# Performance work log

Hardware: AMD Instinct MI355X
Metric: run time of the kernel (lower is better)

The kernel has to match this reference:

```python
import jax, jax.numpy as jnp
import numpy as np

# PercentClosenessBoosting (not in provided source): standard form is
#   new_boost = boost_tensor + (1 - tensor / tensor.max()) * boost_percent
# i.e. units far from the max get boosted more.

def _fwd_math(x, boost_tensor, sparsity, boost_percent):
    B, E = x.shape
    # --- run_boosting ---
    new_boost = boost_tensor + (1.0 - x / jnp.max(x)) * boost_percent
    boosted = jnp.maximum(x, 0.0) + new_boost
    # inhibition tensor starts empty -> apply_sparse_self_affector is a no-op
    # --- run_k_winners_positive: top-k (max_active) per row of boosted, binarize ---
    order = jnp.argsort(-boosted, axis=1)          # descending sort indices
    rank = jnp.argsort(order, axis=1)              # rank of each element in its row
    max_active = jnp.ceil(sparsity[1] * E)
    saved = jnp.where((rank < max_active) & (boosted > 0), 1.0, 0.0)  # ctx.save_for_backward
    # --- choose_boosted_to_satisfy_minimum (note: GLOBAL sum vs per-row min, faithful) ---
    min_active = jnp.floor(sparsity[0] * E)
    active = jnp.sum(saved)
    to_activate = jnp.ceil(min_active - active)
    border = jnp.argsort(-new_boost, axis=1)
    brank = jnp.argsort(border, axis=1)
    need = active < min_active
    out = jnp.where(need & (brank < to_activate), 1.0, saved)
    # --- zero boost where active ---
    final_boost = jnp.where(out > 0, jnp.zeros_like(new_boost), new_boost)
    return out, final_boost, saved


def setup_inputs() -> dict:
    key = jax.random.key(0)
    k1, = jax.random.split(key, 1)
    B, E = 64, 131072
    x = jax.random.normal(k1, (B, E), dtype=jnp.float32)
    boost_tensor = jnp.zeros((B, E), dtype=jnp.float32)
    sparsity = jnp.array([0.002, 0.02], dtype=jnp.float32)
    boost_percent = jnp.float32(1e-8)
    return {"x": x, "boost_tensor": boost_tensor, "sparsity": sparsity, "boost_percent": boost_percent}


def reference(x, boost_tensor, sparsity, boost_percent):
    out, final_boost, _ = _fwd_math(x, boost_tensor, sparsity, boost_percent)
    return out, final_boost
```

## Files before the change

### kernel.cpp

```cpp
#include <hip/hip_runtime.h>

#define BR 64
#define EC 131072
#define CAP 8192
#define LCAP 1024
#define CHUNKS 16
#define CHUNK_V (EC / CHUNKS / 4)
#define NSCH 41
#define NS (NSCH * 64)
#define SSTRIDE 3197
#define BINS 4096

typedef float nf4 __attribute__((ext_vector_type(4)));

#define WS_GMAX 0
#define WS_TOACT 2
#define WS_UT 136
#define WS_CUT 200
#define WS_CCNT 264
#define WS_UT2 512
#define WS_CUT2 576
#define WS_NPOS 640
#define WS_BMAX 1024
#define CAND_U_OFF 4096
#define CAND_I_OFF (CAND_U_OFF + BR * CAP)

__device__ __forceinline__ unsigned map_f(float f) {
    unsigned b = __float_as_uint(f);
    return (b & 0x80000000u) ? ~b : (b | 0x80000000u);
}
__device__ __forceinline__ float unmap_f(unsigned u) {
    unsigned b = (u & 0x80000000u) ? (u & 0x7FFFFFFFu) : ~u;
    return __uint_as_float(b);
}

__device__ __forceinline__ void compute_vals(float x, float bt, float gmax, float bp,
                                             float* nb, float* bo) {
#pragma clang fp contract(off)
    float q = x / gmax;
    float t = 1.0f - q;
    float p = t * bp;
    float nbv = bt + p;
    *nb = nbv;
    *bo = fmaxf(x, 0.0f) + nbv;
}

__device__ __forceinline__ unsigned umax_(unsigned a, unsigned b) { return a > b ? a : b; }
__device__ __forceinline__ unsigned umin_(unsigned a, unsigned b) { return a < b ? a : b; }

__device__ __forceinline__ unsigned calc_K(const float* sp) {
    unsigned K = (unsigned)ceilf(sp[1] * (float)EC);
    if (K > EC) K = EC;
    if (K == 0) K = 1;
    return K;
}

__device__ unsigned lds_radix_select(const unsigned* su, unsigned n, unsigned K,
                                     unsigned* hist, unsigned* scan, unsigned* sb,
                                     int t, unsigned* krem) {
    unsigned pv = 0, Kp = K;
    for (int pass = 0; pass < 4; ++pass) {
        int shift = 24 - 8 * pass;
        hist[t] = 0;
        __syncthreads();
        for (unsigned i = t; i < n; i += 256) {
            unsigned u = su[i];
            bool match = (pass == 0) || ((u >> (shift + 8)) == (pv >> (shift + 8)));
            if (match) atomicAdd(&hist[(u >> shift) & 0xFFu], 1u);
        }
        __syncthreads();
        unsigned my = hist[t];
        scan[t] = my;
        __syncthreads();
        for (int off = 1; off < 256; off <<= 1) {
            unsigned v = (t + off < 256) ? scan[t + off] : 0u;
            __syncthreads();
            scan[t] += v;
            __syncthreads();
        }
        unsigned incl = scan[t], excl = incl - my;
        if (excl < Kp && incl >= Kp) {
            sb[0] = pv | ((unsigned)t << shift);
            sb[1] = Kp - excl;
        }
        __syncthreads();
        pv = sb[0];
        Kp = sb[1];
        __syncthreads();
    }
    *krem = Kp;
    return pv;
}

template<int USE_NB>
__device__ unsigned row_select_full(const float* xr, const float* br, float gmax,
                                    float bp, unsigned K, unsigned* hist,
                                    unsigned* aux, int t,
                                    unsigned* ut_out, unsigned* cut_out) {
    unsigned prefix = 0, Kp = K;
    for (int pass = 0; pass < 4; ++pass) {
        int shift = 24 - 8 * pass;
        hist[t] = 0;
        __syncthreads();
        for (int i = t; i < EC; i += 256) {
            float nb, bo;
            compute_vals(xr[i], br[i], gmax, bp, &nb, &bo);
            unsigned u = map_f(USE_NB ? nb : bo);
            bool match = (pass == 0) || ((u >> (shift + 8)) == (prefix >> (shift + 8)));
            if (match) atomicAdd(&hist[(u >> shift) & 0xFFu], 1u);
        }
        __syncthreads();
        if (t == 0) {
            unsigned cum = 0, bsel = 0, kr = Kp;
            for (int b = 255; b >= 0; --b) {
                unsigned h = hist[b];
                if (cum + h >= Kp) { bsel = (unsigned)b; kr = Kp - cum; break; }
                cum += h;
            }
            aux[0] = prefix | (bsel << shift);
            aux[1] = kr;
        }
        __syncthreads();
        prefix = aux[0];
        Kp = aux[1];
        __syncthreads();
    }
    unsigned u_t = prefix, ties = Kp;
    if (t == 0) { aux[6] = 0; aux[7] = 0xFFFFFFFFu; }
    __syncthreads();
    int wid = t >> 6, lane = t & 63;
    for (int base0 = 0; base0 < EC; base0 += 256) {
        int i = base0 + t;
        float nb, bo;
        compute_vals(xr[i], br[i], gmax, bp, &nb, &bo);
        bool eq = (map_f(USE_NB ? nb : bo) == u_t);
        unsigned long long bal = __ballot(eq);
        if (lane == 0) aux[2 + wid] = (unsigned)__popcll(bal);
        __syncthreads();
        unsigned run = aux[6];
        unsigned wpre = 0;
        for (int w = 0; w < wid; ++w) wpre += aux[2 + w];
        if (eq) {
            unsigned r = run + wpre + (unsigned)__popcll(bal & ((1ull << lane) - 1ull));
            if (r == ties - 1) aux[7] = (unsigned)i;
        }
        __syncthreads();
        if (t == 0) aux[6] = run + aux[2] + aux[3] + aux[4] + aux[5];
        __syncthreads();
        if (aux[6] >= ties) break;
    }
    if (t == 0) { *ut_out = u_t; *cut_out = aux[7]; }
    __syncthreads();
    return u_t;
}

__global__ __launch_bounds__(256) void kA(const float4* __restrict__ x4,
                                          unsigned* __restrict__ ws) {
    if (blockIdx.x == 0)
        for (int i = threadIdx.x; i < 1024; i += 256) ws[i] = 0u;
    unsigned m = 0;
    const int nvec = BR * EC / 4;
    int stride = gridDim.x * 256;
    for (int v = blockIdx.x * 256 + threadIdx.x; v < nvec; v += stride) {
        float4 xv = x4[v];
        m = umax_(m, map_f(xv.x)); m = umax_(m, map_f(xv.y));
        m = umax_(m, map_f(xv.z)); m = umax_(m, map_f(xv.w));
    }
    for (int off = 32; off; off >>= 1) m = umax_(m, __shfl_down(m, off, 64));
    __shared__ unsigned sm[4];
    if ((threadIdx.x & 63) == 0) sm[threadIdx.x >> 6] = m;
    __syncthreads();
    if (threadIdx.x == 0)
        ws[WS_BMAX + blockIdx.x] = umax_(umax_(sm[0], sm[1]), umax_(sm[2], sm[3]));
}

__global__ __launch_bounds__(256) void kB(const float* __restrict__ x,
                                          const float* __restrict__ bt,
                                          const float* __restrict__ sp,
                                          const float* __restrict__ bp_p,
                                          unsigned* __restrict__ ws) {
    __shared__ unsigned hist[BINS];
    __shared__ unsigned lu[LCAP], li[LCAP];
    __shared__ unsigned ssum[256], sabove[256];
    __shared__ unsigned sred[4];
    __shared__ unsigned stlo, slcnt, sgbase;
    int t = threadIdx.x;
    int row = blockIdx.x >> 4, chunk = blockIdx.x & (CHUNKS - 1);

    unsigned m = 0;
    for (int i = t; i < 1024; i += 256) m = umax_(m, ws[WS_BMAX + i]);
    for (int off = 32; off; off >>= 1) m = umax_(m, __shfl_down(m, off, 64));
    if ((t & 63) == 0) sred[t >> 6] = m;
    __syncthreads();
    unsigned gmu = umax_(umax_(sred[0], sred[1]), umax_(sred[2], sred[3]));
    if (blockIdx.x == 0 && t == 0) ws[WS_GMAX] = gmu;
    float gmax = unmap_f(gmu);
    float bp = *bp_p;

    for (int i = t; i < BINS; i += 256) hist[i] = 0;
    if (t == 0) slcnt = 0;
    __syncthreads();
    const float* xr = x + (size_t)row * EC;
    const float* br = bt + (size_t)row * EC;
    for (int s = t; s < NS; s += 256) {
        int idx = (s >> 6) * SSTRIDE + (s & 63);
        float nb, bo;
        compute_vals(xr[idx], br[idx], gmax, bp, &nb, &bo);
        atomicAdd(&hist[map_f(bo) >> 20], 1u);
    }
    __syncthreads();

    unsigned K = calc_K(sp);
    unsigned R = (unsigned)ceilf(1.75f * (float)NS * (float)K / (float)EC);
    if (R < 32) R = 32;
    if (R > NS) R = NS;
    unsigned hv[16];
    unsigned s = 0;
    #pragma unroll
    for (int j = 0; j < 16; ++j) { hv[j] = hist[t * 16 + j]; s += hv[j]; }
    ssum[t] = s;
    __syncthreads();
    if (t == 0) {
        unsigned acc = 0;
        for (int q = 255; q >= 0; --q) { sabove[q] = acc; acc += ssum[q]; }
    }
    __syncthreads();
    unsigned cum = sabove[t];
    for (int j = 15; j >= 0; --j) {
        unsigned h = hv[j];
        if (cum < R && cum + h >= R) stlo = ((unsigned)(t * 16 + j)) << 20;
        cum += h;
    }
    __syncthreads();
    unsigned tlo = stlo ? stlo - 1u : 0u;

    const float4* x4 = (const float4*)x;
    const float4* bt4 = (const float4*)bt;
    unsigned* cu = ws + CAND_U_OFF + (size_t)row * CAP;
    unsigned* ci = ws + CAND_I_OFF + (size_t)row * CAP;
    size_t base = (size_t)row * (EC / 4) + (size_t)chunk * CHUNK_V;
    int ebase = chunk * (EC / CHUNKS);
    unsigned posc = 0;
    for (int v = t; v < CHUNK_V; v += 256) {
        float4 xv = x4[base + v];
        float4 bv = bt4[base + v];
        float xs[4] = {xv.x, xv.y, xv.z, xv.w};
        float bs[4] = {bv.x, bv.y, bv.z, bv.w};
        #pragma unroll
        for (int j = 0; j < 4; ++j) {
            float nb, bo;
            compute_vals(xs[j], bs[j], gmax, bp, &nb, &bo);
            unsigned u = map_f(bo);
            posc += (u > 0x80000000u) ? 1u : 0u;
            if (u > tlo) {
                unsigned p = atomicAdd(&slcnt, 1u);
                if (p < LCAP) {
                    lu[p] = u; li[p] = (unsigned)(ebase + v * 4 + j);
                } else {
                    unsigned gp = atomicAdd(&ws[WS_CCNT + row], 1u);
                    if (gp < CAP) { cu[gp] = u; ci[gp] = (unsigned)(ebase + v * 4 + j); }
                }
            }
        }
    }
    for (int off = 32; off; off >>= 1) posc += __shfl_down(posc, off, 64);
    if ((t & 63) == 0) sred[t >> 6] = posc;
    __syncthreads();
    if (t == 0) atomicAdd(&ws[WS_NPOS + row], sred[0] + sred[1] + sred[2] + sred[3]);
    __syncthreads();
    unsigned n = slcnt < LCAP ? slcnt : LCAP;
    if (t == 0) sgbase = atomicAdd(&ws[WS_CCNT + row], n);
    __syncthreads();
    unsigned gb = sgbase;
    for (unsigned i = t; i < n; i += 256) {
        unsigned gp = gb + i;
        if (gp < CAP) { cu[gp] = lu[i]; ci[gp] = li[i]; }
    }
}

__global__ __launch_bounds__(256) void kC(const float* __restrict__ x,
                                          const float* __restrict__ bt,
                                          const float* __restrict__ sp,
                                          const float* __restrict__ bp_p,
                                          unsigned* __restrict__ ws) {
    int row = blockIdx.x;
    int t = threadIdx.x;
    unsigned n = ws[WS_CCNT + row];
    unsigned K = calc_K(sp);
    float gmax = unmap_f(ws[WS_GMAX]);
    float bp = *bp_p;
    __shared__ unsigned su[CAP];
    __shared__ unsigned hist[256], scan[256], sb[2];
    __shared__ unsigned marr[256];
    __shared__ unsigned mcnt;
    __shared__ unsigned aux[8];
    __shared__ unsigned sact;
    if (n >= K && n <= CAP) {
        const unsigned* cu = ws + CAND_U_OFF + (size_t)row * CAP;
        const unsigned* ci = ws + CAND_I_OFF + (size_t)row * CAP;
        for (unsigned i = t; i < n; i += 256) su[i] = cu[i];
        if (t == 0) mcnt = 0;
        __syncthreads();
        unsigned krem2;
        unsigned u_t = lds_radix_select(su, n, K, hist, scan, sb, t, &krem2);
        for (unsigned i = t; i < n; i += 256)
            if (su[i] == u_t) {
                unsigned p = atomicAdd(&mcnt, 1u);
                if (p < 256) marr[p] = ci[i];
            }
        __syncthreads();
        unsigned m = mcnt;
        if (m <= 256) {
            for (unsigned i = t; i < m; i += 256) {
                unsigned myidx = marr[i];
                unsigned r = 0;
                for (unsigned j = 0; j < m; ++j) r += (marr[j] < myidx) ? 1u : 0u;
                if (r == krem2 - 1) { ws[WS_UT + row] = u_t; ws[WS_CUT + row] = myidx; }
            }
        } else {
            for (unsigned i = t; i < n; i += 256) {
                if (su[i] == u_t) {
                    unsigned myidx = ci[i];
                    unsigned r = 0;
                    for (unsigned j = 0; j < n; ++j)
                        if (su[j] == u_t && ci[j] < myidx) ++r;
                    if (r == krem2 - 1) { ws[WS_UT + row] = u_t; ws[WS_CUT + row] = myidx; }
                }
            }
        }
    } else {
        row_select_full<0>(x + (size_t)row * EC, bt + (size_t)row * EC, gmax, bp, K,
                           hist, aux, t, &ws[WS_UT + row], &ws[WS_CUT + row]);
    }

    unsigned act = 0;
    if (t < 64) act = umin_(K, ws[WS_NPOS + t]);
    for (int off = 32; off; off >>= 1) act += __shfl_down(act, off, 64);
    if (t == 0) sact = act;
    __syncthreads();
    float active = (float)sact;
    float min_active = floorf(sp[0] * (float)EC);
    if (active < min_active) {
        unsigned K2 = (unsigned)ceilf(min_active - active);
        if (row == 0 && t == 0) ws[WS_TOACT] = K2;
        if (K2 > EC) K2 = EC;
        row_select_full<1>(x + (size_t)row * EC, bt + (size_t)row * EC, gmax, bp, K2,
                           hist, aux, t, &ws[WS_UT2 + row], &ws[WS_CUT2 + row]);
    }
}

__global__ void kE(const float4* __restrict__ x4, const float4* __restrict__ bt4,
                   const float* __restrict__ bp_p, const unsigned* __restrict__ ws,
                   nf4* __restrict__ out4, nf4* __restrict__ fb4) {
    float gmax = unmap_f(ws[WS_GMAX]);
    float bp = *bp_p;
    unsigned toact = ws[WS_TOACT];
    const size_t nvec = (size_t)BR * EC / 4;
    size_t stride = (size_t)gridDim.x * blockDim.x;
    for (size_t v = (size_t)blockIdx.x * blockDim.x + threadIdx.x; v < nvec; v += stride) {
        size_t e0 = v << 2;
        int row = (int)(e0 >> 17);
        int col = (int)(e0 & (size_t)(EC - 1));
        unsigned u_t = ws[WS_UT + row];
        int cut = (int)ws[WS_CUT + row];
        float4 xv = x4[v], bv = bt4[v];
        float xarr[4] = {xv.x, xv.y, xv.z, xv.w};
        float barr[4] = {bv.x, bv.y, bv.z, bv.w};
        nf4 o, f;
        #pragma unroll
        for (int j = 0; j < 4; ++j) {
            float nb, bo;
            compute_vals(xarr[j], barr[j], gmax, bp, &nb, &bo);
            unsigned u = map_f(bo);
            bool sel = (u > u_t) || ((u == u_t) && ((col + j) <= cut));
            bool saved = sel && (u > 0x80000000u);
            o[j] = saved ? 1.0f : 0.0f;
            f[j] = saved ? 0.0f : nb;
        }
        if (toact) {
            unsigned ut2 = ws[WS_UT2 + row];
            int cut2 = (int)ws[WS_CUT2 + row];
            #pragma unroll
            for (int j = 0; j < 4; ++j) {
                float nb, bo;
                compute_vals(xarr[j], barr[j], gmax, bp, &nb, &bo);
                unsigned u2 = map_f(nb);
                if (u2 > ut2 || (u2 == ut2 && (col + j) <= cut2)) {
                    o[j] = 1.0f;
                    f[j] = 0.0f;
                }
            }
        }
        __builtin_nontemporal_store(o, &out4[v]);
        __builtin_nontemporal_store(f, &fb4[v]);
    }
}

extern "C" void kernel_launch(void* const* d_in, const int* in_sizes, int n_in,
                              void* d_out, int out_size, void* d_ws, size_t ws_size,
                              hipStream_t stream) {
    const float* x  = (const float*)d_in[0];
    const float* bt = (const float*)d_in[1];
    const float* sp = (const float*)d_in[2];
    const float* bp = (const float*)d_in[3];
    float* out = (float*)d_out;
    float* fb  = out + (size_t)BR * EC;
    unsigned* ws = (unsigned*)d_ws;

    kA<<<1024, 256, 0, stream>>>((const float4*)x, ws);
    kB<<<BR * CHUNKS, 256, 0, stream>>>(x, bt, sp, bp, ws);
    kC<<<BR, 256, 0, stream>>>(x, bt, sp, bp, ws);
    kE<<<2048, 256, 0, stream>>>((const float4*)x, (const float4*)bt, bp, ws,
                                 (nf4*)out, (nf4*)fb);
}
```

Baseline: 76.69 us.

## Fuse output write into candidate pass and scatter winners, drop final kernel

The kernel that writes the output and the final boost is removed. The candidate-collection kernel now writes default zeros and the new_boost values while it streams x and boost_tensor. The selection kernel then scatters 1/0 only at the selected winner indices, so a full extra read of both inputs is avoided. The fallback and minimum-activation paths still run full-row scans inside the per-row kernel with scalar scattered stores. These paths run on only 64 blocks, which could be slow if they trigger.

```diff
diff --git a/kernel.cpp b/kernel.cpp
--- a/kernel.cpp
+++ b/kernel.cpp
@@ -14,12 +14,7 @@
 typedef float nf4 __attribute__((ext_vector_type(4)));
 
 #define WS_GMAX 0
-#define WS_TOACT 2
-#define WS_UT 136
-#define WS_CUT 200
 #define WS_CCNT 264
-#define WS_UT2 512
-#define WS_CUT2 576
 #define WS_NPOS 640
 #define WS_BMAX 1024
 #define CAND_U_OFF 4096
@@ -95,8 +90,7 @@
 template<int USE_NB>
 __device__ unsigned row_select_full(const float* xr, const float* br, float gmax,
                                     float bp, unsigned K, unsigned* hist,
-                                    unsigned* aux, int t,
-                                    unsigned* ut_out, unsigned* cut_out) {
+                                    unsigned* aux, int t, unsigned* cut_out) {
     unsigned prefix = 0, Kp = K;
     for (int pass = 0; pass < 4; ++pass) {
         int shift = 24 - 8 * pass;
@@ -149,7 +143,7 @@
         __syncthreads();
         if (aux[6] >= ties) break;
     }
-    if (t == 0) { *ut_out = u_t; *cut_out = aux[7]; }
+    if (t == 0) *cut_out = aux[7];
     __syncthreads();
     return u_t;
 }
@@ -178,7 +172,9 @@
                                           const float* __restrict__ bt,
                                           const float* __restrict__ sp,
                                           const float* __restrict__ bp_p,
-                                          unsigned* __restrict__ ws) {
+                                          unsigned* __restrict__ ws,
+                                          nf4* __restrict__ out4,
+                                          nf4* __restrict__ fb4) {
     __shared__ unsigned hist[BINS];
     __shared__ unsigned lu[LCAP], li[LCAP];
     __shared__ unsigned ssum[256], sabove[256];
@@ -240,17 +236,20 @@
     unsigned* ci = ws + CAND_I_OFF + (size_t)row * CAP;
     size_t base = (size_t)row * (EC / 4) + (size_t)chunk * CHUNK_V;
     int ebase = chunk * (EC / CHUNKS);
+    const nf4 zo = {0.0f, 0.0f, 0.0f, 0.0f};
     unsigned posc = 0;
     for (int v = t; v < CHUNK_V; v += 256) {
         float4 xv = x4[base + v];
         float4 bv = bt4[base + v];
         float xs[4] = {xv.x, xv.y, xv.z, xv.w};
         float bs[4] = {bv.x, bv.y, bv.z, bv.w};
+        nf4 fv;
         #pragma unroll
         for (int j = 0; j < 4; ++j) {
             float nb, bo;
             compute_vals(xs[j], bs[j], gmax, bp, &nb, &bo);
             unsigned u = map_f(bo);
+            fv[j] = nb;
             posc += (u > 0x80000000u) ? 1u : 0u;
             if (u > tlo) {
                 unsigned p = atomicAdd(&slcnt, 1u);
@@ -262,6 +261,8 @@
                 }
             }
         }
+        __builtin_nontemporal_store(zo, &out4[base + v]);
+        __builtin_nontemporal_store(fv, &fb4[base + v]);
     }
     for (int off = 32; off; off >>= 1) posc += __shfl_down(posc, off, 64);
     if ((t & 63) == 0) sred[t >> 6] = posc;
@@ -282,19 +283,25 @@
                                           const float* __restrict__ bt,
                                           const float* __restrict__ sp,
                                           const float* __restrict__ bp_p,
-                                          unsigned* __restrict__ ws) {
+                                          unsigned* __restrict__ ws,
+                                          float* __restrict__ out,
+                                          float* __restrict__ fb) {
     int row = blockIdx.x;
     int t = threadIdx.x;
     unsigned n = ws[WS_CCNT + row];
     unsigned K = calc_K(sp);
     float gmax = unmap_f(ws[WS_GMAX]);
     float bp = *bp_p;
+    const float* xr = x + (size_t)row * EC;
+    const float* br = bt + (size_t)row * EC;
+    float* outr = out + (size_t)row * EC;
+    float* fbr = fb + (size_t)row * EC;
     __shared__ unsigned su[CAP];
     __shared__ unsigned hist[256], scan[256], sb[2];
     __shared__ unsigned marr[256];
     __shared__ unsigned mcnt;
     __shared__ unsigned aux[8];
-    __shared__ unsigned sact;
+    __shared__ unsigned sact, scut;
     if (n >= K && n <= CAP) {
         const unsigned* cu = ws + CAND_U_OFF + (size_t)row * CAP;
         const unsigned* ci = ws + CAND_I_OFF + (size_t)row * CAP;
@@ -315,7 +322,7 @@
                 unsigned myidx = marr[i];
                 unsigned r = 0;
                 for (unsigned j = 0; j < m; ++j) r += (marr[j] < myidx) ? 1u : 0u;
-                if (r == krem2 - 1) { ws[WS_UT + row] = u_t; ws[WS_CUT + row] = myidx; }
+                if (r == krem2 - 1) scut = myidx;
             }
         } else {
             for (unsigned i = t; i < n; i += 256) {
@@ -324,13 +331,27 @@
                     unsigned r = 0;
                     for (unsigned j = 0; j < n; ++j)
                         if (su[j] == u_t && ci[j] < myidx) ++r;
-                    if (r == krem2 - 1) { ws[WS_UT + row] = u_t; ws[WS_CUT + row] = myidx; }
+                    if (r == krem2 - 1) scut = myidx;
                 }
             }
         }
+        __syncthreads();
+        unsigned cut = scut;
+        for (unsigned i = t; i < n; i += 256) {
+            unsigned u = su[i], idx = ci[i];
+            bool sel = (u > u_t) || ((u == u_t) && (idx <= cut));
+            if (sel && u > 0x80000000u) { outr[idx] = 1.0f; fbr[idx] = 0.0f; }
+        }
     } else {
-        row_select_full<0>(x + (size_t)row * EC, bt + (size_t)row * EC, gmax, bp, K,
-                           hist, aux, t, &ws[WS_UT + row], &ws[WS_CUT + row]);
+        unsigned u_t = row_select_full<0>(xr, br, gmax, bp, K, hist, aux, t, &scut);
+        unsigned cut = scut;
+        for (int i = t; i < EC; i += 256) {
+            float nb, bo;
+            compute_vals(xr[i], br[i], gmax, bp, &nb, &bo);
+            unsigned u = map_f(bo);
+            bool sel = (u > u_t) || ((u == u_t) && ((unsigned)i <= cut));
+            if (sel && u > 0x80000000u) { outr[i] = 1.0f; fbr[i] = 0.0f; }
+        }
     }
 
     unsigned act = 0;
@@ -342,57 +363,18 @@
     float min_active = floorf(sp[0] * (float)EC);
     if (active < min_active) {
         unsigned K2 = (unsigned)ceilf(min_active - active);
-        if (row == 0 && t == 0) ws[WS_TOACT] = K2;
         if (K2 > EC) K2 = EC;
-        row_select_full<1>(x + (size_t)row * EC, bt + (size_t)row * EC, gmax, bp, K2,
-                           hist, aux, t, &ws[WS_UT2 + row], &ws[WS_CUT2 + row]);
-    }
-}
-
-__global__ void kE(const float4* __restrict__ x4, const float4* __restrict__ bt4,
-                   const float* __restrict__ bp_p, const unsigned* __restrict__ ws,
-                   nf4* __restrict__ out4, nf4* __restrict__ fb4) {
-    float gmax = unmap_f(ws[WS_GMAX]);
-    float bp = *bp_p;
-    unsigned toact = ws[WS_TOACT];
-    const size_t nvec = (size_t)BR * EC / 4;
-    size_t stride = (size_t)gridDim.x * blockDim.x;
-    for (size_t v = (size_t)blockIdx.x * blockDim.x + threadIdx.x; v < nvec; v += stride) {
-        size_t e0 = v << 2;
-        int row = (int)(e0 >> 17);
-        int col = (int)(e0 & (size_t)(EC - 1));
-        unsigned u_t = ws[WS_UT + row];
-        int cut = (int)ws[WS_CUT + row];
-        float4 xv = x4[v], bv = bt4[v];
-        float xarr[4] = {xv.x, xv.y, xv.z, xv.w};
-        float barr[4] = {bv.x, bv.y, bv.z, bv.w};
-        nf4 o, f;
-        #pragma unroll
-        for (int j = 0; j < 4; ++j) {
+        unsigned ut2 = row_select_full<1>(xr, br, gmax, bp, K2, hist, aux, t, &scut);
+        unsigned cut2 = scut;
+        for (int i = t; i < EC; i += 256) {
             float nb, bo;
-            compute_vals(xarr[j], barr[j], gmax, bp, &nb, &bo);
-            unsigned u = map_f(bo);
-            bool sel = (u > u_t) || ((u == u_t) && ((col + j) <= cut));
-            bool saved = sel && (u > 0x80000000u);
-            o[j] = saved ? 1.0f : 0.0f;
-            f[j] = saved ? 0.0f : nb;
-        }
-        if (toact) {
-            unsigned ut2 = ws[WS_UT2 + row];
-            int cut2 = (int)ws[WS_CUT2 + row];
-            #pragma unroll
-            for (int j = 0; j < 4; ++j) {
-                float nb, bo;
-                compute_vals(xarr[j], barr[j], gmax, bp, &nb, &bo);
-                unsigned u2 = map_f(nb);
-                if (u2 > ut2 || (u2 == ut2 && (col + j) <= cut2)) {
-                    o[j] = 1.0f;
-                    f[j] = 0.0f;
-                }
-            }
-        }
-        __builtin_nontemporal_store(o, &out4[v]);
-        __builtin_nontemporal_store(f, &fb4[v]);
+            compute_vals(xr[i], br[i], gmax, bp, &nb, &bo);
+            unsigned u2 = map_f(nb);
+            if (u2 > ut2 || (u2 == ut2 && (unsigned)i <= cut2)) {
+                outr[i] = 1.0f;
+                fbr[i] = 0.0f;
+            }
+        }
     }
 }
 
@@ -408,8 +390,6 @@
     unsigned* ws = (unsigned*)d_ws;
 
     kA<<<1024, 256, 0, stream>>>((const float4*)x, ws);
-    kB<<<BR * CHUNKS, 256, 0, stream>>>(x, bt, sp, bp, ws);
-    kC<<<BR, 256, 0, stream>>>(x, bt, sp, bp, ws);
-    kE<<<2048, 256, 0, stream>>>((const float4*)x, (const float4*)bt, bp, ws,
-                                 (nf4*)out, (nf4*)fb);
-}
+    kB<<<BR * CHUNKS, 256, 0, stream>>>(x, bt, sp, bp, ws, (nf4*)out, (nf4*)fb);
+    kC<<<BR, 256, 0, stream>>>(x, bt, sp, bp, ws, out, fb);
+}
```

Result: faster. 74.76 us (-2.5%).
